# Optimization experiments

Measured on AMD Instinct MI355X. Metric: run time of the kernel, lower is better.

## Reference

```python
import jax, jax.numpy as jnp
import numpy as np

S, P, C = 64, 2048, 32   # num_scenes, num_pixels, scene_channels
A, D, E = 2048, 128, 64  # agent_size, dynamics_features, embed_dim


def setup_inputs() -> dict:
    key = jax.random.key(0)
    ks = jax.random.split(key, 9)
    inv = lambda n: 1.0 / np.sqrt(n)
    return {
        "global_scene": jax.random.normal(ks[0], (S, P, C), jnp.float32),
        "scene_idx": jax.random.randint(ks[1], (A,), 0, S),
        "dynamic_encoding": jax.random.normal(ks[2], (A, D), jnp.float32),
        "W_sn": jax.random.uniform(ks[3], (C, E), jnp.float32, -inv(C), inv(C)),
        "b_sn": jax.random.uniform(ks[4], (E,), jnp.float32, -inv(C), inv(C)),
        "W_df": jax.random.uniform(ks[5], (D, E), jnp.float32, -inv(D), inv(D)),
        "b_df": jax.random.uniform(ks[6], (E,), jnp.float32, -inv(D), inv(D)),
        "w_fc": jax.random.uniform(ks[7], (E,), jnp.float32, -inv(E), inv(E)),
        "b_fc": jax.random.uniform(ks[8], (1,), jnp.float32, -inv(E), inv(E)),
    }


def reference(global_scene, scene_idx, dynamic_encoding, W_sn, b_sn, W_df, b_df, w_fc, b_fc):
    # att1: [S, P, E]; att2: [A, E]
    att1 = jnp.einsum('spc,ce->spe', global_scene, W_sn) + b_sn
    att2 = dynamic_encoding @ W_df + b_df
    # gather scenes per agent, fuse add + relu: [A, P, E]
    add_fusion = jax.nn.relu(att1[scene_idx] + att2[:, None, :])
    # linear to scalar score per pixel, softmax over pixels (dim=1)
    logits = jnp.einsum('ape,e->ap', add_fusion, w_fc) + b_fc[0]  # [A, P]
    alpha = jax.nn.softmax(logits, axis=1)[:, :, None]            # [A, P, 1]
    # alpha-weighted pooling of gathered scene features -> [A, C]
    return jnp.sum(alpha * global_scene[scene_idx], axis=1)
```

## Files before the change

kernel.cpp:

```cpp
#include <hip/hip_runtime.h>
#include <hip/hip_bf16.h>

#define S_ 64
#define P_ 2048
#define C_ 32
#define A_ 2048
#define D_ 128
#define E_ 64

#define LPX   128
#define NLCH  (P_ / LPX)

__global__ __launch_bounds__(256) void att2s_kernel(
    const float* __restrict__ de, const float* __restrict__ Wdf,
    const float* __restrict__ bdf, const int* __restrict__ sidx,
    float* __restrict__ att2, int* __restrict__ counts,
    int* __restrict__ lists, float* __restrict__ out, float* __restrict__ Z) {
  __shared__ float4 Wl[128 * 16];
  __shared__ float4 bl[16];
  __shared__ float  dl[16 * 128];
  const int tid = threadIdx.x;

  {
    const float4 z4 = make_float4(0.f, 0.f, 0.f, 0.f);
    const int gidx = blockIdx.x * 256 + tid;
    if (gidx < (A_ * C_) / 4)      ((float4*)out)[gidx] = z4;
    else if (gidx < (A_ * C_) / 4 + A_ / 4)
      ((float4*)Z)[gidx - (A_ * C_) / 4] = z4;
  }

  if (tid < 16) {
    const int a = blockIdx.x * 16 + tid;
    const int s = sidx[a];
    const int pos = atomicAdd(&counts[s], 1);
    lists[s * A_ + pos] = a;
  }

  const float4* W4 = (const float4*)Wdf;
#pragma unroll
  for (int i = 0; i < 8; ++i) Wl[tid + i * 256] = W4[tid + i * 256];
  if (tid < 16) bl[tid] = ((const float4*)bdf)[tid];
  const long base = (long)blockIdx.x * (16 * 128);
#pragma unroll
  for (int i = 0; i < 8; ++i) dl[tid + i * 256] = de[base + tid + i * 256];
  __syncthreads();

  const int r = tid >> 4, e4 = tid & 15;
  float4 acc = bl[e4];
#pragma unroll 4
  for (int d = 0; d < 128; ++d) {
    const float  g = dl[r * 128 + d];
    const float4 w = Wl[d * 16 + e4];
    acc.x = fmaf(g, w.x, acc.x);
    acc.y = fmaf(g, w.y, acc.y);
    acc.z = fmaf(g, w.z, acc.z);
    acc.w = fmaf(g, w.w, acc.w);
  }
  ((float4*)att2)[((long)blockIdx.x * 16 + r) * 16 + e4] = acc;
}

__global__ __launch_bounds__(256) void fused_kernel(
    const float* __restrict__ gs, const float* __restrict__ Wsn,
    const float* __restrict__ bsn, const float* __restrict__ wfc,
    const float* __restrict__ att2, const int* __restrict__ counts,
    const int* __restrict__ lists, float* __restrict__ out,
    float* __restrict__ Z) {
  const int s   = blockIdx.x >> 4;
  const int p0  = (blockIdx.x & (NLCH - 1)) * LPX;
  const int tid = threadIdx.x;
  const int px  = tid >> 1;
  const int eh  = tid & 1;

  __shared__ float  gsl[LPX][36];
  __shared__ float4 Wl4[32 * 16];
  __shared__ float4 a2l[32][16];
  __shared__ float  alpha_l[32][132];
  __shared__ int    aidl[32];

  const float4* W4 = (const float4*)Wsn;
  Wl4[tid]       = W4[tid];
  Wl4[tid + 256] = W4[tid + 256];

  const float4* g4 = (const float4*)(gs + ((long)s * P_ + p0) * C_);
#pragma unroll
  for (int k = 0; k < 4; ++k) {
    const int f = tid + k * 256;
    const float4 v = g4[f];
    const int pp = f >> 3, c0 = (f & 7) * 4;
    gsl[pp][c0]     = v.x;
    gsl[pp][c0 + 1] = v.y;
    gsl[pp][c0 + 2] = v.z;
    gsl[pp][c0 + 3] = v.w;
  }

  const float4* wf4 = (const float4*)wfc;
  const float4* b4  = (const float4*)bsn;
  float4 wf[8], a1[8];
#pragma unroll
  for (int q = 0; q < 8; ++q) { wf[q] = wf4[eh * 8 + q]; a1[q] = b4[eh * 8 + q]; }
  __syncthreads();

#pragma unroll
  for (int c = 0; c < 32; ++c) {
    const float g = gsl[px][c];
#pragma unroll
    for (int q = 0; q < 8; ++q) {
      const float4 w = Wl4[c * 16 + eh * 8 + q];
      a1[q].x = fmaf(g, w.x, a1[q].x);
      a1[q].y = fmaf(g, w.y, a1[q].y);
      a1[q].z = fmaf(g, w.z, a1[q].z);
      a1[q].w = fmaf(g, w.w, a1[q].w);
    }
  }

  const int j2 = tid >> 3;
  const int c4 = tid & 7;
  const int n_s = counts[s];

  for (int g0 = 0; g0 < n_s; g0 += 32) {
    const int m = min(32, n_s - g0);
    __syncthreads();
    if (tid < m) aidl[tid] = lists[s * A_ + g0 + tid];
    __syncthreads();
#pragma unroll
    for (int k = 0; k < 2; ++k) {
      const int idx = tid + k * 256;
      const int j = idx >> 4, e4 = idx & 15;
      if (j < m) a2l[j][e4] = ((const float4*)att2)[aidl[j] * 16 + e4];
    }
    __syncthreads();

    for (int j = 0; j < m; ++j) {
      float c0 = 0.f, c1 = 0.f, c2 = 0.f, c3 = 0.f;
#pragma unroll
      for (int q = 0; q < 8; ++q) {
        const float4 t = a2l[j][eh * 8 + q];
        const float4 w = wf[q];
        const float4 av = a1[q];
        c0 = fmaf(fmaxf(av.x + t.x, 0.f), w.x, c0);
        c1 = fmaf(fmaxf(av.y + t.y, 0.f), w.y, c1);
        c2 = fmaf(fmaxf(av.z + t.z, 0.f), w.z, c2);
        c3 = fmaf(fmaxf(av.w + t.w, 0.f), w.w, c3);
      }
      float r = (c0 + c1) + (c2 + c3);
      r += __shfl_xor(r, 1);
      if (eh == 0) alpha_l[j][px] = __expf(r);
    }
    __syncthreads();

    if (j2 < m) {
      const int a = aidl[j2];
      float4 a0 = make_float4(0.f, 0.f, 0.f, 0.f);
      float4 a1p = make_float4(0.f, 0.f, 0.f, 0.f);
      float4 a2p = make_float4(0.f, 0.f, 0.f, 0.f);
      float4 a3p = make_float4(0.f, 0.f, 0.f, 0.f);
      float  zs = 0.f;
#pragma unroll 4
      for (int p4 = 0; p4 < LPX / 4; ++p4) {
        const float w0 = alpha_l[j2][p4 * 4 + 0];
        const float w1 = alpha_l[j2][p4 * 4 + 1];
        const float w2 = alpha_l[j2][p4 * 4 + 2];
        const float w3 = alpha_l[j2][p4 * 4 + 3];
        const float4 v0 = *(const float4*)&gsl[p4 * 4 + 0][c4 * 4];
        const float4 v1 = *(const float4*)&gsl[p4 * 4 + 1][c4 * 4];
        const float4 v2 = *(const float4*)&gsl[p4 * 4 + 2][c4 * 4];
        const float4 v3 = *(const float4*)&gsl[p4 * 4 + 3][c4 * 4];
        zs += (w0 + w1) + (w2 + w3);
        a0.x = fmaf(w0, v0.x, a0.x); a0.y = fmaf(w0, v0.y, a0.y);
        a0.z = fmaf(w0, v0.z, a0.z); a0.w = fmaf(w0, v0.w, a0.w);
        a1p.x = fmaf(w1, v1.x, a1p.x); a1p.y = fmaf(w1, v1.y, a1p.y);
        a1p.z = fmaf(w1, v1.z, a1p.z); a1p.w = fmaf(w1, v1.w, a1p.w);
        a2p.x = fmaf(w2, v2.x, a2p.x); a2p.y = fmaf(w2, v2.y, a2p.y);
        a2p.z = fmaf(w2, v2.z, a2p.z); a2p.w = fmaf(w2, v2.w, a2p.w);
        a3p.x = fmaf(w3, v3.x, a3p.x); a3p.y = fmaf(w3, v3.y, a3p.y);
        a3p.z = fmaf(w3, v3.z, a3p.z); a3p.w = fmaf(w3, v3.w, a3p.w);
      }
      const float4 acc = make_float4((a0.x + a1p.x) + (a2p.x + a3p.x),
                                     (a0.y + a1p.y) + (a2p.y + a3p.y),
                                     (a0.z + a1p.z) + (a2p.z + a3p.z),
                                     (a0.w + a1p.w) + (a2p.w + a3p.w));
      float* op = out + (long)a * C_ + c4 * 4;
      atomicAdd(op,     acc.x);
      atomicAdd(op + 1, acc.y);
      atomicAdd(op + 2, acc.z);
      atomicAdd(op + 3, acc.w);
      if (c4 == 0) atomicAdd(&Z[a], zs);
    }
  }
}

__global__ __launch_bounds__(256) void norm_kernel(
    float* __restrict__ out, const float* __restrict__ Z) {
  const int i = blockIdx.x * 256 + threadIdx.x;
  out[i] = out[i] / Z[i >> 5];
}

extern "C" void kernel_launch(void* const* d_in, const int* in_sizes, int n_in,
                              void* d_out, int out_size, void* d_ws, size_t ws_size,
                              hipStream_t stream) {
  const float* gs   = (const float*)d_in[0];
  const int*   sidx = (const int*)  d_in[1];
  const float* de   = (const float*)d_in[2];
  const float* Wsn  = (const float*)d_in[3];
  const float* bsn  = (const float*)d_in[4];
  const float* Wdf  = (const float*)d_in[5];
  const float* bdf  = (const float*)d_in[6];
  const float* wfc  = (const float*)d_in[7];
  float* out = (float*)d_out;

  float* att2   = (float*)d_ws;
  float* Z      = att2 + (long)A_ * E_;
  int*   counts = (int*)(Z + A_);
  int*   lists  = counts + 64;

  hipMemsetAsync(counts, 0, 64 * sizeof(int), stream);
  att2s_kernel<<<A_ / 16,   256, 0, stream>>>(de, Wdf, bdf, sidx, att2,
                                              counts, lists, out, Z);
  fused_kernel<<<S_ * NLCH, 256, 0, stream>>>(gs, Wsn, bsn, wfc, att2,
                                              counts, lists, out, Z);
  norm_kernel <<<(A_ * C_) / 256, 256, 0, stream>>>(out, Z);
}
```

Measured before the change: 151.1 us.

## Replace output atomics with per-chunk partial buffers reduced in norm kernel

The fused kernel now writes each agent's pooled result for its pixel chunk into a dedicated partial buffer with a plain float4 store, instead of doing four float atomicAdds into the output. The norm kernel sums the 16 chunk partials and divides by Z, so the output no longer needs zeroing. The goal is to remove atomic contention and serialization on the output. In exchange, about 4 MB of extra partial traffic is written and read back. Separately, the W_sn staging buffer and the alpha buffer now share one shared-memory region to cut LDS use, and agent ids are loaded together with the att2 rows, which drops one barrier per group.

```diff
diff --git a/kernel.cpp b/kernel.cpp
--- a/kernel.cpp
+++ b/kernel.cpp
@@ -15,19 +15,14 @@
     const float* __restrict__ de, const float* __restrict__ Wdf,
     const float* __restrict__ bdf, const int* __restrict__ sidx,
     float* __restrict__ att2, int* __restrict__ counts,
-    int* __restrict__ lists, float* __restrict__ out, float* __restrict__ Z) {
+    int* __restrict__ lists, float* __restrict__ Z) {
   __shared__ float4 Wl[128 * 16];
   __shared__ float4 bl[16];
   __shared__ float  dl[16 * 128];
   const int tid = threadIdx.x;
 
-  {
-    const float4 z4 = make_float4(0.f, 0.f, 0.f, 0.f);
-    const int gidx = blockIdx.x * 256 + tid;
-    if (gidx < (A_ * C_) / 4)      ((float4*)out)[gidx] = z4;
-    else if (gidx < (A_ * C_) / 4 + A_ / 4)
-      ((float4*)Z)[gidx - (A_ * C_) / 4] = z4;
-  }
+  if (blockIdx.x == 0 && tid < A_ / 4)
+    ((float4*)Z)[tid] = make_float4(0.f, 0.f, 0.f, 0.f);
 
   if (tid < 16) {
     const int a = blockIdx.x * 16 + tid;
@@ -63,19 +58,22 @@
     const float* __restrict__ gs, const float* __restrict__ Wsn,
     const float* __restrict__ bsn, const float* __restrict__ wfc,
     const float* __restrict__ att2, const int* __restrict__ counts,
-    const int* __restrict__ lists, float* __restrict__ out,
+    const int* __restrict__ lists, float* __restrict__ partial,
     float* __restrict__ Z) {
   const int s   = blockIdx.x >> 4;
-  const int p0  = (blockIdx.x & (NLCH - 1)) * LPX;
+  const int ch  = blockIdx.x & (NLCH - 1);
+  const int p0  = ch * LPX;
   const int tid = threadIdx.x;
   const int px  = tid >> 1;
   const int eh  = tid & 1;
 
   __shared__ float  gsl[LPX][36];
-  __shared__ float4 Wl4[32 * 16];
+  __shared__ float  ubuf[32 * 132];
   __shared__ float4 a2l[32][16];
-  __shared__ float  alpha_l[32][132];
   __shared__ int    aidl[32];
+
+  float4* Wl4 = (float4*)ubuf;
+  float (*alpha_l)[132] = (float(*)[132])ubuf;
 
   const float4* W4 = (const float4*)Wsn;
   Wl4[tid]       = W4[tid];
@@ -120,13 +118,15 @@
   for (int g0 = 0; g0 < n_s; g0 += 32) {
     const int m = min(32, n_s - g0);
     __syncthreads();
-    if (tid < m) aidl[tid] = lists[s * A_ + g0 + tid];
-    __syncthreads();
 #pragma unroll
     for (int k = 0; k < 2; ++k) {
       const int idx = tid + k * 256;
       const int j = idx >> 4, e4 = idx & 15;
-      if (j < m) a2l[j][e4] = ((const float4*)att2)[aidl[j] * 16 + e4];
+      if (j < m) {
+        const int aj = lists[s * A_ + g0 + j];
+        a2l[j][e4] = ((const float4*)att2)[aj * 16 + e4];
+        if (e4 == 0) aidl[j] = aj;
+      }
     }
     __syncthreads();
 
@@ -179,20 +179,20 @@
                                      (a0.y + a1p.y) + (a2p.y + a3p.y),
                                      (a0.z + a1p.z) + (a2p.z + a3p.z),
                                      (a0.w + a1p.w) + (a2p.w + a3p.w));
-      float* op = out + (long)a * C_ + c4 * 4;
-      atomicAdd(op,     acc.x);
-      atomicAdd(op + 1, acc.y);
-      atomicAdd(op + 2, acc.z);
-      atomicAdd(op + 3, acc.w);
+      *(float4*)(partial + (long)ch * (A_ * C_) + (long)a * C_ + c4 * 4) = acc;
       if (c4 == 0) atomicAdd(&Z[a], zs);
     }
   }
 }
 
 __global__ __launch_bounds__(256) void norm_kernel(
-    float* __restrict__ out, const float* __restrict__ Z) {
+    const float* __restrict__ partial, const float* __restrict__ Z,
+    float* __restrict__ out) {
   const int i = blockIdx.x * 256 + threadIdx.x;
-  out[i] = out[i] / Z[i >> 5];
+  float sum = 0.f;
+#pragma unroll
+  for (int ch = 0; ch < NLCH; ++ch) sum += partial[(long)ch * (A_ * C_) + i];
+  out[i] = sum / Z[i >> 5];
 }
 
 extern "C" void kernel_launch(void* const* d_in, const int* in_sizes, int n_in,
@@ -208,15 +208,16 @@
   const float* wfc  = (const float*)d_in[7];
   float* out = (float*)d_out;
 
-  float* att2   = (float*)d_ws;
-  float* Z      = att2 + (long)A_ * E_;
-  int*   counts = (int*)(Z + A_);
-  int*   lists  = counts + 64;
+  float* att2    = (float*)d_ws;
+  float* Z       = att2 + (long)A_ * E_;
+  int*   counts  = (int*)(Z + A_);
+  int*   lists   = counts + 64;
+  float* partial = (float*)(lists + (long)S_ * A_);
 
   hipMemsetAsync(counts, 0, 64 * sizeof(int), stream);
   att2s_kernel<<<A_ / 16,   256, 0, stream>>>(de, Wdf, bdf, sidx, att2,
-                                              counts, lists, out, Z);
+                                              counts, lists, Z);
   fused_kernel<<<S_ * NLCH, 256, 0, stream>>>(gs, Wsn, bsn, wfc, att2,
-                                              counts, lists, out, Z);
-  norm_kernel <<<(A_ * C_) / 256, 256, 0, stream>>>(out, Z);
-}
+                                              counts, lists, partial, Z);
+  norm_kernel <<<(A_ * C_) / 256, 256, 0, stream>>>(partial, Z, out);
+}
```

Measured after the change: 141.7 us. 6.2% less time.
